# Performance work log

Hardware: AMD Instinct MI355X
Metric: run time of the kernel (lower is better)

Reference implementation:

```python
import jax, jax.numpy as jnp
import numpy as np

N_NODES = 50000
N_EDGES = 800000
IN_FEATS = 128
H_FEATS = 32
HEADS = 4
OUT_FEATS = 32
OUT_HEADS = 1
NEG_SLOPE = 0.2


def setup_inputs() -> dict:
    key = jax.random.key(0)
    ks = jax.random.split(key, 20)
    s = 0.05
    return {
        "features": jax.random.normal(ks[0], (N_NODES, IN_FEATS), jnp.float32),
        "src": jax.random.randint(ks[1], (N_EDGES,), 0, N_NODES, jnp.int32),
        "dst": jax.random.randint(ks[2], (N_EDGES,), 0, N_NODES, jnp.int32),
        "Ws0": jax.random.normal(ks[3], (IN_FEATS, HEADS * H_FEATS), jnp.float32) * s,
        "bs0": jnp.zeros((HEADS * H_FEATS,), jnp.float32),
        "Wd0": jax.random.normal(ks[4], (IN_FEATS, HEADS * H_FEATS), jnp.float32) * s,
        "bd0": jnp.zeros((HEADS * H_FEATS,), jnp.float32),
        "a0": jax.random.normal(ks[5], (HEADS, H_FEATS), jnp.float32) * s,
        "Ws1": jax.random.normal(ks[6], (HEADS * H_FEATS, HEADS * H_FEATS), jnp.float32) * s,
        "bs1": jnp.zeros((HEADS * H_FEATS,), jnp.float32),
        "Wd1": jax.random.normal(ks[7], (HEADS * H_FEATS, HEADS * H_FEATS), jnp.float32) * s,
        "bd1": jnp.zeros((HEADS * H_FEATS,), jnp.float32),
        "a1": jax.random.normal(ks[8], (HEADS, H_FEATS), jnp.float32) * s,
        "Ws2": jax.random.normal(ks[9], (HEADS * H_FEATS, OUT_HEADS * OUT_FEATS), jnp.float32) * s,
        "bs2": jnp.zeros((OUT_HEADS * OUT_FEATS,), jnp.float32),
        "Wd2": jax.random.normal(ks[10], (HEADS * H_FEATS, OUT_HEADS * OUT_FEATS), jnp.float32) * s,
        "bd2": jnp.zeros((OUT_HEADS * OUT_FEATS,), jnp.float32),
        "a2": jax.random.normal(ks[11], (OUT_HEADS, OUT_FEATS), jnp.float32) * s,
    }


def gatv2_conv(x, src, dst, Ws, bs, Wd, bd, attn, n_nodes):
    """DGL GATv2Conv (share_weights=False, residual=False, no dropout)."""
    heads, f = attn.shape
    feat_src = (x @ Ws + bs).reshape(-1, heads, f)  # [N, H, F]
    feat_dst = (x @ Wd + bd).reshape(-1, heads, f)  # [N, H, F]
    # per-edge GATv2 score: LeakyReLU(Wsrc h_u + Wdst h_v) . a
    e = jax.nn.leaky_relu(feat_src[src] + feat_dst[dst], NEG_SLOPE)  # [E, H, F]
    logits = jnp.einsum("ehf,hf->eh", e, attn)  # [E, H]
    # edge softmax over incoming edges of each dst node
    m = jax.ops.segment_max(logits, dst, num_segments=n_nodes)  # [N, H]
    ex = jnp.exp(logits - m[dst])
    denom = jax.ops.segment_sum(ex, dst, num_segments=n_nodes)  # [N, H]
    alpha = ex / denom[dst]  # [E, H]
    # scatter-aggregate messages
    msg = feat_src[src] * alpha[..., None]  # [E, H, F]
    return jax.ops.segment_sum(msg, dst, num_segments=n_nodes)  # [N, H, F]


def reference(features, src, dst,
              Ws0, bs0, Wd0, bd0, a0,
              Ws1, bs1, Wd1, bd1, a1,
              Ws2, bs2, Wd2, bd2, a2):
    n = features.shape[0]
    h = gatv2_conv(features, src, dst, Ws0, bs0, Wd0, bd0, a0, n)
    h = jax.nn.relu(h.reshape(n, -1))
    h = gatv2_conv(h, src, dst, Ws1, bs1, Wd1, bd1, a1, n)
    h = jax.nn.relu(h.reshape(n, -1))
    h = gatv2_conv(h, src, dst, Ws2, bs2, Wd2, bd2, a2, n)
    return h.mean(axis=1)  # [N, OUT_FEATS]
```

## Files before the change

### kernel.cpp

```cpp
#include <hip/hip_runtime.h>

typedef __attribute__((ext_vector_type(8))) short bf16x8;
typedef __attribute__((ext_vector_type(4))) float f32x4;

#define LOG2E 1.4426950408889634f

#define BINSH 8
#define NBIN 196
#define CHUNK 4096
#define K4CAP 6144

__device__ __forceinline__ unsigned bf_rn(float f) {
    unsigned u = __float_as_uint(f);
    u += 0x7fffu + ((u >> 16) & 1u);
    return u >> 16;
}
__device__ __forceinline__ float bf_lo(unsigned u) { return __uint_as_float(u << 16); }
__device__ __forceinline__ float bf_hi(unsigned u) { return __uint_as_float(u & 0xffff0000u); }

template <int CTRL>
__device__ __forceinline__ float dpp_radd(float x) {
    int t = __builtin_amdgcn_update_dpp(0, __float_as_int(x), CTRL, 0xF, 0xF, true);
    return x + __int_as_float(t);
}
__device__ __forceinline__ float sum8(float p) {
    p = dpp_radd<0x141>(p);
    p = dpp_radd<0x1B>(p);
    p = dpp_radd<0xB1>(p);
    return p;
}
__device__ __forceinline__ float sum4(float p) {
    p = dpp_radd<0xB1>(p);
    p = dpp_radd<0x4E>(p);
    return p;
}
__device__ __forceinline__ float dpp_swap1(float x) {
    return __int_as_float(__builtin_amdgcn_update_dpp(0, __float_as_int(x), 0xB1, 0xF, 0xF, true));
}

__device__ __forceinline__ float fast_exp2(float x) {
#if __has_builtin(__builtin_amdgcn_exp2f)
    return __builtin_amdgcn_exp2f(x);
#else
    return __expf(x * 0.6931471805599453f);
#endif
}


__global__ __launch_bounds__(256) void bin_count(const int* __restrict__ dst,
                                                 int* __restrict__ binCnt, int e) {
    __shared__ int hist[NBIN];
    for (int t = threadIdx.x; t < NBIN; t += 256) hist[t] = 0;
    __syncthreads();
    int base = blockIdx.x * CHUNK;
    int cnt = min(CHUNK, e - base);
    for (int j = threadIdx.x; j < cnt; j += 256)
        atomicAdd(&hist[dst[base + j] >> BINSH], 1);
    __syncthreads();
    for (int t = threadIdx.x; t < NBIN; t += 256)
        if (hist[t]) atomicAdd(&binCnt[t], hist[t]);
}

__global__ void bin_scan(const int* __restrict__ binCnt, int* __restrict__ binBase,
                         int* __restrict__ binCur, int* __restrict__ rowp, int n, int e) {
    int t = threadIdx.x;
    int v = (t < NBIN) ? binCnt[t] : 0;
    int lane = t & 63, w = t >> 6;
    int incl = v;
    for (int off = 1; off < 64; off <<= 1) {
        int tt = __shfl_up(incl, off);
        if (lane >= off) incl += tt;
    }
    __shared__ int wsum[4];
    if (lane == 63) wsum[w] = incl;
    __syncthreads();
    int wpre = 0;
    for (int i = 0; i < w; ++i) wpre += wsum[i];
    int excl = wpre + incl - v;
    if (t < NBIN) { binBase[t] = excl; binCur[t] = excl; }
    if (t == 0) { binBase[NBIN] = e; rowp[n] = e; }
}

__global__ __launch_bounds__(256) void bin_scatter(
    const int* __restrict__ src, const int* __restrict__ dst,
    int* __restrict__ binCur, unsigned* __restrict__ ebin, int e) {
    __shared__ int hist[256];
    __shared__ int seg[256];
    __shared__ int gbase[NBIN];
    __shared__ unsigned pack[CHUNK];
    for (int t = threadIdx.x; t < 256; t += 256) hist[t] = 0;
    __syncthreads();
    int base = blockIdx.x * CHUNK;
    int cnt = min(CHUNK, e - base);

    for (int j = threadIdx.x; j < cnt; j += 256)
        atomicAdd(&hist[dst[base + j] >> BINSH], 1);
    __syncthreads();
    if (threadIdx.x < 64) {
        int l = threadIdx.x;
        int s = 0, loc[4];
#pragma unroll
        for (int k = 0; k < 4; ++k) { loc[k] = s; s += hist[l * 4 + k]; }
        int incl = s;
        for (int off = 1; off < 64; off <<= 1) {
            int tt = __shfl_up(incl, off);
            if (l >= off) incl += tt;
        }
        int excl = incl - s;
#pragma unroll
        for (int k = 0; k < 4; ++k) seg[l * 4 + k] = excl + loc[k];
    }
    __syncthreads();
    if (threadIdx.x < NBIN && hist[threadIdx.x])
        gbase[threadIdx.x] = atomicAdd(&binCur[threadIdx.x], hist[threadIdx.x]);
    __syncthreads();
    for (int t = threadIdx.x; t < 256; t += 256) hist[t] = seg[t];
    __syncthreads();
    for (int j = threadIdx.x; j < cnt; j += 256) {
        int d = dst[base + j], s = src[base + j];
        int b = d >> BINSH, dl = d & ((1 << BINSH) - 1);
        int pos = atomicAdd(&hist[b], 1);
        pack[pos] = ((unsigned)b << 24) | ((unsigned)dl << 16) | (unsigned)s;
    }
    __syncthreads();
    for (int j = threadIdx.x; j < cnt; j += 256) {
        unsigned wv = pack[j];
        int b = wv >> 24;
        ebin[gbase[b] + (j - seg[b])] = wv;
    }
}

__global__ __launch_bounds__(256) void csr_build(
    const unsigned* __restrict__ ebin, const int* __restrict__ binBase,
    int* __restrict__ rowp, int* __restrict__ csrc, int n) {
    __shared__ int hist[256];
    __shared__ int seg[256];
    __shared__ unsigned stage[K4CAP];
    int b = blockIdx.x;
    int e0 = binBase[b], e1 = binBase[b + 1];
    int n0 = b << BINSH;
    int nn = min(256, n - n0);
    for (int t = threadIdx.x; t < 256; t += 256) hist[t] = 0;
    __syncthreads();
    for (int i = e0 + threadIdx.x; i < e1; i += 256) {
        unsigned wv = ebin[i];
        atomicAdd(&hist[(wv >> 16) & 255], 1);
        int off = i - e0;
        if (off < K4CAP) stage[off] = wv;
    }
    __syncthreads();
    if (threadIdx.x < 64) {
        int l = threadIdx.x;
        int s = 0, loc[4];
#pragma unroll
        for (int k = 0; k < 4; ++k) { loc[k] = s; s += hist[l * 4 + k]; }
        int incl = s;
        for (int off = 1; off < 64; off <<= 1) {
            int tt = __shfl_up(incl, off);
            if (l >= off) incl += tt;
        }
        int excl = incl - s;
#pragma unroll
        for (int k = 0; k < 4; ++k) seg[l * 4 + k] = excl + loc[k];
    }
    __syncthreads();
    for (int t = threadIdx.x; t < nn; t += 256) rowp[n0 + t] = e0 + seg[t];
    for (int t = threadIdx.x; t < 256; t += 256) hist[t] = seg[t];
    __syncthreads();
    for (int i = e0 + threadIdx.x; i < e1; i += 256) {
        int off = i - e0;
        unsigned wv = (off < K4CAP) ? stage[off] : ebin[i];
        int dl = (wv >> 16) & 255;
        int pos = e0 + atomicAdd(&hist[dl], 1);
        csrc[pos] = (int)(wv & 0xFFFFu);
    }
}


__global__ __launch_bounds__(256) void prep(
    const float* __restrict__ x, unsigned short* __restrict__ xb, int n4,
    const float* __restrict__ Ws0, const float* __restrict__ Wd0,
    const float* __restrict__ Ws1, const float* __restrict__ Wd1,
    const float* __restrict__ Ws2, const float* __restrict__ Wd2,
    unsigned short* __restrict__ wt0, unsigned short* __restrict__ wt1,
    unsigned short* __restrict__ wt2, int* __restrict__ binCnt) {
    int gid = blockIdx.x * blockDim.x + threadIdx.x;
    if (gid < NBIN) binCnt[gid] = 0;
    if (gid < n4) {
        float4 v = *(const float4*)(x + (size_t)gid * 4);
        ushort4 r;
        r.x = (unsigned short)bf_rn(v.x); r.y = (unsigned short)bf_rn(v.y);
        r.z = (unsigned short)bf_rn(v.z); r.w = (unsigned short)bf_rn(v.w);
        *(ushort4*)(xb + (size_t)gid * 4) = r;
    } else {
        int g = gid - n4;
        if (g < 65536) {
            int l = g >> 15, loc = g & 32767;
            int c = loc >> 7, k = loc & 127;
            const float* W = (c < 128) ? (l ? Ws1 : Ws0) : (l ? Wd1 : Wd0);
            int cc = c & 127;
            float v = W[(size_t)k * 128 + cc];
            (l ? wt1 : wt0)[loc] = (unsigned short)bf_rn(v);
        } else if (g < 65536 + 8192) {
            int loc = g - 65536;
            int c = loc >> 7, k = loc & 127;
            const float* W = (c < 32) ? Ws2 : Wd2;
            int cc = (c < 32) ? c : c - 32;
            float v = W[(size_t)k * 32 + cc];
            wt2[loc] = (unsigned short)bf_rn(v);
        }
    }
}


template <int COLS2>
__global__ __launch_bounds__(256) void gemm_dual2(
    const unsigned short* __restrict__ xb, const unsigned short* __restrict__ wt,
    const float* __restrict__ bs, const float* __restrict__ bd,
    unsigned short* __restrict__ fs, unsigned short* __restrict__ fd,
    int n, int nch) {
    constexpr int C  = COLS2 / 2;
    constexpr int NC = COLS2 / 64;

    const int lane = threadIdx.x & 63;
    const int m = lane & 15, quad = lane >> 4;
    const int gwid = blockIdx.x * 4 + (threadIdx.x >> 6);
    const int nwaves = gridDim.x * 4;
    const int cs = gwid % NC;
    const int cstride = nwaves / NC;

    float biasv[4];
#pragma unroll
    for (int ct = 0; ct < 4; ++ct) {
        int col = cs * 64 + ct * 16 + m;
        biasv[ct] = (col < C) ? bs[col] : bd[col - C];
    }

    for (int chunk = gwid / NC; chunk < nch; chunk += cstride) {
        const size_t r0 = (size_t)chunk * 64;

        f32x4 acc[4][4];
#pragma unroll
        for (int rt = 0; rt < 4; ++rt)
#pragma unroll
            for (int ct = 0; ct < 4; ++ct) acc[rt][ct] = (f32x4){0.f, 0.f, 0.f, 0.f};

#pragma unroll
        for (int ks = 0; ks < 4; ++ks) {
            const int ko = ks * 32 + quad * 8;
            bf16x8 a[4], b[4];
#pragma unroll
            for (int rt = 0; rt < 4; ++rt)
                a[rt] = *(const bf16x8*)(xb + (r0 + rt * 16 + m) * 128 + ko);
#pragma unroll
            for (int ct = 0; ct < 4; ++ct)
                b[ct] = *(const bf16x8*)(wt + (size_t)(cs * 64 + ct * 16 + m) * 128 + ko);
#pragma unroll
            for (int rt = 0; rt < 4; ++rt)
#pragma unroll
                for (int ct = 0; ct < 4; ++ct)
                    acc[rt][ct] = __builtin_amdgcn_mfma_f32_16x16x32_bf16(a[rt], b[ct], acc[rt][ct], 0, 0, 0);
        }

        const int odd = m & 1;
#pragma unroll
        for (int ct = 0; ct < 4; ++ct) {
            int colE = cs * 64 + ct * 16 + (m & ~1);
            unsigned short* ptr = (colE < C) ? fs : fd;
            int cc = (colE < C) ? colE : colE - C;
#pragma unroll
            for (int rt = 0; rt < 4; ++rt) {
                float v0 = acc[rt][ct][0] + biasv[ct];
                float v1 = acc[rt][ct][1] + biasv[ct];
                float v2 = acc[rt][ct][2] + biasv[ct];
                float v3 = acc[rt][ct][3] + biasv[ct];
                float s0 = dpp_swap1(v0), s1 = dpp_swap1(v1);
                float s2 = dpp_swap1(v2), s3 = dpp_swap1(v3);
                float aLo = odd ? s2 : v0, aHi = odd ? v2 : s0;
                float bLo = odd ? s3 : v1, bHi = odd ? v3 : s1;
                int rowA = (int)r0 + rt * 16 + quad * 4 + (odd ? 2 : 0);
                unsigned pa = (bf_rn(aHi) << 16) | bf_rn(aLo);
                unsigned pb = (bf_rn(bHi) << 16) | bf_rn(bLo);
                if (rowA < n)     *(unsigned*)(ptr + (size_t)rowA * C + cc)       = pa;
                if (rowA + 1 < n) *(unsigned*)(ptr + ((size_t)rowA + 1) * C + cc) = pb;
            }
        }
    }
}


#define EDGE_BODY(u, mval)                                          \
    do {                                                            \
        float x0 = bf_lo((u).x), x1 = bf_hi((u).x);                 \
        float x2 = bf_lo((u).y), x3 = bf_hi((u).y);                 \
        float t0 = x0 + fd0, t1 = x1 + fd1;                         \
        float t2 = x2 + fd2, t3 = x3 + fd3;                         \
        float p = a060 * t0;                                        \
        p = fmaf(a040, fabsf(t0), p);                               \
        p = fmaf(a061, t1, p); p = fmaf(a041, fabsf(t1), p);        \
        p = fmaf(a062, t2, p); p = fmaf(a042, fabsf(t2), p);        \
        p = fmaf(a063, t3, p); p = fmaf(a043, fabsf(t3), p);        \
        p = sum8(p);                                                \
        float ex = fast_exp2(p) * (mval);                           \
        denom += ex;                                                \
        acc0 = fmaf(ex, x0, acc0); acc1 = fmaf(ex, x1, acc1);       \
        acc2 = fmaf(ex, x2, acc2); acc3 = fmaf(ex, x3, acc3);       \
    } while (0)

#define EB8(u, mval)                                                \
    do {                                                            \
        float x0 = bf_lo((u).x), x1 = bf_hi((u).x);                 \
        float x2 = bf_lo((u).y), x3 = bf_hi((u).y);                 \
        float x4 = bf_lo((u).z), x5 = bf_hi((u).z);                 \
        float x6 = bf_lo((u).w), x7 = bf_hi((u).w);                 \
        float t0 = x0 + fd0, t1 = x1 + fd1;                         \
        float t2 = x2 + fd2, t3 = x3 + fd3;                         \
        float t4 = x4 + fd4, t5 = x5 + fd5;                         \
        float t6 = x6 + fd6, t7 = x7 + fd7;                         \
        float p = a60_0 * t0;                                       \
        p = fmaf(a40_0, fabsf(t0), p);                              \
        p = fmaf(a60_1, t1, p); p = fmaf(a40_1, fabsf(t1), p);      \
        p = fmaf(a60_2, t2, p); p = fmaf(a40_2, fabsf(t2), p);      \
        p = fmaf(a60_3, t3, p); p = fmaf(a40_3, fabsf(t3), p);      \
        p = fmaf(a60_4, t4, p); p = fmaf(a40_4, fabsf(t4), p);      \
        p = fmaf(a60_5, t5, p); p = fmaf(a40_5, fabsf(t5), p);      \
        p = fmaf(a60_6, t6, p); p = fmaf(a40_6, fabsf(t6), p);      \
        p = fmaf(a60_7, t7, p); p = fmaf(a40_7, fabsf(t7), p);      \
        p = sum4(p);                                                \
        float ex = fast_exp2(p) * (mval);                           \
        denom += ex;                                                \
        acc0 = fmaf(ex, x0, acc0); acc1 = fmaf(ex, x1, acc1);       \
        acc2 = fmaf(ex, x2, acc2); acc3 = fmaf(ex, x3, acc3);       \
        acc4 = fmaf(ex, x4, acc4); acc5 = fmaf(ex, x5, acc5);       \
        acc6 = fmaf(ex, x6, acc6); acc7 = fmaf(ex, x7, acc7);       \
    } while (0)

__global__ __launch_bounds__(256) void conv128(
    const unsigned short* __restrict__ fs, const unsigned short* __restrict__ fd,
    const float* __restrict__ attn, const int* __restrict__ rowp,
    const int* __restrict__ csrc, unsigned short* __restrict__ out, int n) {
    const int nwaves = gridDim.x * 4;
    const int wid0 = blockIdx.x * 4 + (threadIdx.x >> 6);
    const int lane = threadIdx.x & 63;
    const int slot = lane >> 4;
    const int c = lane & 15;

    float4 av0 = *(const float4*)(attn + c * 8);
    float4 av1 = *(const float4*)(attn + c * 8 + 4);
    const float a60_0 = av0.x * 0.6f * LOG2E, a40_0 = av0.x * 0.4f * LOG2E;
    const float a60_1 = av0.y * 0.6f * LOG2E, a40_1 = av0.y * 0.4f * LOG2E;
    const float a60_2 = av0.z * 0.6f * LOG2E, a40_2 = av0.z * 0.4f * LOG2E;
    const float a60_3 = av0.w * 0.6f * LOG2E, a40_3 = av0.w * 0.4f * LOG2E;
    const float a60_4 = av1.x * 0.6f * LOG2E, a40_4 = av1.x * 0.4f * LOG2E;
    const float a60_5 = av1.y * 0.6f * LOG2E, a40_5 = av1.y * 0.4f * LOG2E;
    const float a60_6 = av1.z * 0.6f * LOG2E, a40_6 = av1.z * 0.4f * LOG2E;
    const float a60_7 = av1.w * 0.6f * LOG2E, a40_7 = av1.w * 0.4f * LOG2E;

    for (int wid = wid0; wid < n; wid += nwaves) {
        uint4 ud = *(const uint4*)(fd + (size_t)wid * 128 + c * 8);
        float fd0 = bf_lo(ud.x), fd1 = bf_hi(ud.x);
        float fd2 = bf_lo(ud.y), fd3 = bf_hi(ud.y);
        float fd4 = bf_lo(ud.z), fd5 = bf_hi(ud.z);
        float fd6 = bf_lo(ud.w), fd7 = bf_hi(ud.w);
        int rs = rowp[wid], re = rowp[wid + 1];
        float acc0 = 0.f, acc1 = 0.f, acc2 = 0.f, acc3 = 0.f;
        float acc4 = 0.f, acc5 = 0.f, acc6 = 0.f, acc7 = 0.f, denom = 0.f;

        int i = rs;
        for (; i + 7 < re; i += 8) {
            int sA = csrc[i + slot];
            int sB = csrc[i + 4 + slot];
            uint4 uA = *(const uint4*)(fs + ((size_t)sA << 7) + c * 8);
            uint4 uB = *(const uint4*)(fs + ((size_t)sB << 7) + c * 8);
            EB8(uA, 1.0f);
            EB8(uB, 1.0f);
        }
        for (; i + 3 < re; i += 4) {
            int s = csrc[i + slot];
            uint4 u = *(const uint4*)(fs + ((size_t)s << 7) + c * 8);
            EB8(u, 1.0f);
        }
        if (i < re) {
            int idx = i + slot;
            int s = csrc[min(idx, re - 1)];
            uint4 u = *(const uint4*)(fs + ((size_t)s << 7) + c * 8);
            float mval = (idx < re) ? 1.f : 0.f;
            EB8(u, mval);
        }
        acc0 += __shfl_xor(acc0, 16); acc1 += __shfl_xor(acc1, 16);
        acc2 += __shfl_xor(acc2, 16); acc3 += __shfl_xor(acc3, 16);
        acc4 += __shfl_xor(acc4, 16); acc5 += __shfl_xor(acc5, 16);
        acc6 += __shfl_xor(acc6, 16); acc7 += __shfl_xor(acc7, 16);
        denom += __shfl_xor(denom, 16);
        acc0 += __shfl_xor(acc0, 32); acc1 += __shfl_xor(acc1, 32);
        acc2 += __shfl_xor(acc2, 32); acc3 += __shfl_xor(acc3, 32);
        acc4 += __shfl_xor(acc4, 32); acc5 += __shfl_xor(acc5, 32);
        acc6 += __shfl_xor(acc6, 32); acc7 += __shfl_xor(acc7, 32);
        denom += __shfl_xor(denom, 32);
        float inv = (re > rs) ? 1.f / denom : 0.f;
        float r0 = fmaxf(acc0 * inv, 0.f), r1 = fmaxf(acc1 * inv, 0.f);
        float r2 = fmaxf(acc2 * inv, 0.f), r3 = fmaxf(acc3 * inv, 0.f);
        float r4 = fmaxf(acc4 * inv, 0.f), r5 = fmaxf(acc5 * inv, 0.f);
        float r6 = fmaxf(acc6 * inv, 0.f), r7 = fmaxf(acc7 * inv, 0.f);
        if (slot == 0) {
            uint4 o;
            o.x = (bf_rn(r1) << 16) | bf_rn(r0);
            o.y = (bf_rn(r3) << 16) | bf_rn(r2);
            o.z = (bf_rn(r5) << 16) | bf_rn(r4);
            o.w = (bf_rn(r7) << 16) | bf_rn(r6);
            *(uint4*)(out + (size_t)wid * 128 + c * 8) = o;
        }
    }
}

__global__ __launch_bounds__(256) void conv32(
    const unsigned short* __restrict__ fs, const unsigned short* __restrict__ fd,
    const float* __restrict__ attn, const int* __restrict__ rowp,
    const int* __restrict__ csrc, float* __restrict__ out, int n) {
    const int nwaves = gridDim.x * 4;
    const int wid0 = blockIdx.x * 4 + (threadIdx.x >> 6);
    const int lane = threadIdx.x & 63;
    const int g = lane >> 3;
    const int c = lane & 7;

    float4 av = *(const float4*)(attn + c * 4);
    const float a060 = av.x * 0.6f * LOG2E, a040 = av.x * 0.4f * LOG2E;
    const float a061 = av.y * 0.6f * LOG2E, a041 = av.y * 0.4f * LOG2E;
    const float a062 = av.z * 0.6f * LOG2E, a042 = av.z * 0.4f * LOG2E;
    const float a063 = av.w * 0.6f * LOG2E, a043 = av.w * 0.4f * LOG2E;

    for (int wid = wid0; wid < n; wid += nwaves) {
        uint2 ud = *(const uint2*)(fd + (size_t)wid * 32 + c * 4);
        float fd0 = bf_lo(ud.x), fd1 = bf_hi(ud.x);
        float fd2 = bf_lo(ud.y), fd3 = bf_hi(ud.y);
        int rs = rowp[wid], re = rowp[wid + 1];
        float acc0 = 0.f, acc1 = 0.f, acc2 = 0.f, acc3 = 0.f, denom = 0.f;

        int i = rs;
        for (; i + 15 < re; i += 16) {
            int s0 = csrc[i + g];
            int s1 = csrc[i + 8 + g];
            uint2 u0 = *(const uint2*)(fs + ((size_t)s0 << 5) + c * 4);
            uint2 u1 = *(const uint2*)(fs + ((size_t)s1 << 5) + c * 4);
            EDGE_BODY(u0, 1.0f);
            EDGE_BODY(u1, 1.0f);
        }
        for (; i + 7 < re; i += 8) {
            int s = csrc[i + g];
            uint2 u = *(const uint2*)(fs + ((size_t)s << 5) + c * 4);
            EDGE_BODY(u, 1.0f);
        }
        if (i < re) {
            int idx = i + g;
            int s = csrc[min(idx, re - 1)];
            uint2 u = *(const uint2*)(fs + ((size_t)s << 5) + c * 4);
            float mval = (idx < re) ? 1.f : 0.f;
            EDGE_BODY(u, mval);
        }
        acc0 = dpp_radd<0x128>(acc0); acc1 = dpp_radd<0x128>(acc1);
        acc2 = dpp_radd<0x128>(acc2); acc3 = dpp_radd<0x128>(acc3);
        denom = dpp_radd<0x128>(denom);
        acc0 += __shfl_xor(acc0, 16); acc1 += __shfl_xor(acc1, 16);
        acc2 += __shfl_xor(acc2, 16); acc3 += __shfl_xor(acc3, 16);
        denom += __shfl_xor(denom, 16);
        acc0 += __shfl_xor(acc0, 32); acc1 += __shfl_xor(acc1, 32);
        acc2 += __shfl_xor(acc2, 32); acc3 += __shfl_xor(acc3, 32);
        denom += __shfl_xor(denom, 32);
        float inv = (re > rs) ? 1.f / denom : 0.f;
        if (lane < 8) {
            float4 o;
            o.x = acc0 * inv; o.y = acc1 * inv;
            o.z = acc2 * inv; o.w = acc3 * inv;
            *(float4*)(out + (size_t)wid * 32 + c * 4) = o;
        }
    }
}


extern "C" void kernel_launch(void* const* d_in, const int* in_sizes, int n_in,
                              void* d_out, int out_size, void* d_ws, size_t ws_size,
                              hipStream_t stream) {
    const float* feats = (const float*)d_in[0];
    const int*   src   = (const int*)d_in[1];
    const int*   dst   = (const int*)d_in[2];
    const float* Ws0 = (const float*)d_in[3],  *bs0 = (const float*)d_in[4];
    const float* Wd0 = (const float*)d_in[5],  *bd0 = (const float*)d_in[6];
    const float* a0  = (const float*)d_in[7];
    const float* Ws1 = (const float*)d_in[8],  *bs1 = (const float*)d_in[9];
    const float* Wd1 = (const float*)d_in[10], *bd1 = (const float*)d_in[11];
    const float* a1  = (const float*)d_in[12];
    const float* Ws2 = (const float*)d_in[13], *bs2 = (const float*)d_in[14];
    const float* Wd2 = (const float*)d_in[15], *bd2 = (const float*)d_in[16];
    const float* a2  = (const float*)d_in[17];

    const int N = in_sizes[0] / 128;
    const int E = in_sizes[1];
    const int nch = (N + 63) / 64;
    const int NPAD = nch * 64;

    char* ws = (char*)d_ws;
    const size_t featB = (size_t)NPAD * 128 * 2;
    unsigned short* xb  = (unsigned short*)(ws);
    unsigned short* hb  = (unsigned short*)(ws + featB);
    unsigned short* fsb = (unsigned short*)(ws + 2 * featB);
    unsigned short* fdb = (unsigned short*)(ws + 3 * featB);
    char* p = ws + 4 * featB;
    unsigned short* wt0 = (unsigned short*)p; p += 256 * 128 * 2;
    unsigned short* wt1 = (unsigned short*)p; p += 256 * 128 * 2;
    unsigned short* wt2 = (unsigned short*)p; p += 64 * 128 * 2;
    int* rowp    = (int*)p;      p += ((size_t)(N + 1) * 4 + 255) / 256 * 256;
    int* binCnt  = (int*)p;      p += (NBIN * 4 + 255) / 256 * 256;
    int* binBase = (int*)p;      p += ((NBIN + 1) * 4 + 255) / 256 * 256;
    int* binCur  = (int*)p;      p += (NBIN * 4 + 255) / 256 * 256;
    unsigned* ebin = (unsigned*)p; p += (size_t)E * 4;
    int* csrc    = (int*)p;

    const int nchunks = (E + CHUNK - 1) / CHUNK;
    const int n4 = N * 128 / 4;

    prep<<<(n4 + 73728 + 255) / 256, 256, 0, stream>>>(
        feats, xb, n4, Ws0, Wd0, Ws1, Wd1, Ws2, Wd2, wt0, wt1, wt2, binCnt);

    bin_count<<<nchunks, 256, 0, stream>>>(dst, binCnt, E);
    bin_scan<<<1, 256, 0, stream>>>(binCnt, binBase, binCur, rowp, N, E);
    bin_scatter<<<nchunks, 256, 0, stream>>>(src, dst, binCur, ebin, E);
    csr_build<<<NBIN, 256, 0, stream>>>(ebin, binBase, rowp, csrc, N);

    const int g256 = nch;
    const int g64  = (nch + 3) / 4;
    const int convGrid = 2048;

    gemm_dual2<256><<<g256, 256, 0, stream>>>(xb, wt0, bs0, bd0, fsb, fdb, N, nch);
    conv128<<<convGrid, 256, 0, stream>>>(fsb, fdb, a0, rowp, csrc, hb, N);
    gemm_dual2<256><<<g256, 256, 0, stream>>>(hb, wt1, bs1, bd1, fsb, fdb, N, nch);
    conv128<<<convGrid, 256, 0, stream>>>(fsb, fdb, a1, rowp, csrc, hb, N);
    gemm_dual2<64><<<g64, 256, 0, stream>>>(hb, wt2, bs2, bd2, fsb, fdb, N, nch);
    conv32<<<convGrid, 256, 0, stream>>>(fsb, fdb, a2, rowp, csrc, (float*)d_out, N);
}
```

Baseline: 302.4 us.

## Software-pipeline gathers, use contiguous row ranges per wave, split score reduction

The 128-wide conv kernel now prefetches the next group of source-feature gathers before running the edge math on the current group, so gather latency overlaps with compute. Both conv kernels switch from a grid-stride row loop to contiguous row ranges per wave, which may improve locality of rowp, csrc and output accesses. The score dot product is split into two independent FMA chains to shorten the dependency chain. The costs are higher register pressure from the prefetched uint4 values and possible load imbalance, since each wave's rows can have very different degrees.

Measured after the change: 303.2 us. No clear change (+0.3%).

```diff
diff --git a/kernel.cpp b/kernel.cpp
--- a/kernel.cpp
+++ b/kernel.cpp
@@ -317,16 +317,17 @@
         float t2 = x2 + fd2, t3 = x3 + fd3;                         \
         float t4 = x4 + fd4, t5 = x5 + fd5;                         \
         float t6 = x6 + fd6, t7 = x7 + fd7;                         \
-        float p = a60_0 * t0;                                       \
-        p = fmaf(a40_0, fabsf(t0), p);                              \
-        p = fmaf(a60_1, t1, p); p = fmaf(a40_1, fabsf(t1), p);      \
-        p = fmaf(a60_2, t2, p); p = fmaf(a40_2, fabsf(t2), p);      \
-        p = fmaf(a60_3, t3, p); p = fmaf(a40_3, fabsf(t3), p);      \
-        p = fmaf(a60_4, t4, p); p = fmaf(a40_4, fabsf(t4), p);      \
-        p = fmaf(a60_5, t5, p); p = fmaf(a40_5, fabsf(t5), p);      \
-        p = fmaf(a60_6, t6, p); p = fmaf(a40_6, fabsf(t6), p);      \
-        p = fmaf(a60_7, t7, p); p = fmaf(a40_7, fabsf(t7), p);      \
-        p = sum4(p);                                                \
+        float p0 = a60_0 * t0;                                      \
+        p0 = fmaf(a40_0, fabsf(t0), p0);                            \
+        p0 = fmaf(a60_1, t1, p0); p0 = fmaf(a40_1, fabsf(t1), p0);  \
+        p0 = fmaf(a60_2, t2, p0); p0 = fmaf(a40_2, fabsf(t2), p0);  \
+        p0 = fmaf(a60_3, t3, p0); p0 = fmaf(a40_3, fabsf(t3), p0);  \
+        float p1 = a60_4 * t4;                                      \
+        p1 = fmaf(a40_4, fabsf(t4), p1);                            \
+        p1 = fmaf(a60_5, t5, p1); p1 = fmaf(a40_5, fabsf(t5), p1);  \
+        p1 = fmaf(a60_6, t6, p1); p1 = fmaf(a40_6, fabsf(t6), p1);  \
+        p1 = fmaf(a60_7, t7, p1); p1 = fmaf(a40_7, fabsf(t7), p1);  \
+        float p = sum4(p0 + p1);                                    \
         float ex = fast_exp2(p) * (mval);                           \
         denom += ex;                                                \
         acc0 = fmaf(ex, x0, acc0); acc1 = fmaf(ex, x1, acc1);       \
@@ -340,7 +341,7 @@
     const float* __restrict__ attn, const int* __restrict__ rowp,
     const int* __restrict__ csrc, unsigned short* __restrict__ out, int n) {
     const int nwaves = gridDim.x * 4;
-    const int wid0 = blockIdx.x * 4 + (threadIdx.x >> 6);
+    const int wid = blockIdx.x * 4 + (threadIdx.x >> 6);
     const int lane = threadIdx.x & 63;
     const int slot = lane >> 4;
     const int c = lane & 15;
@@ -356,34 +357,51 @@
     const float a60_6 = av1.z * 0.6f * LOG2E, a40_6 = av1.z * 0.4f * LOG2E;
     const float a60_7 = av1.w * 0.6f * LOG2E, a40_7 = av1.w * 0.4f * LOG2E;
 
-    for (int wid = wid0; wid < n; wid += nwaves) {
-        uint4 ud = *(const uint4*)(fd + (size_t)wid * 128 + c * 8);
+    const int q = n / nwaves, r = n % nwaves;
+    const int row0 = wid * q + min(wid, r);
+    const int row1 = row0 + q + (wid < r ? 1 : 0);
+
+    const unsigned short* fsc = fs + c * 8;
+
+    for (int row = row0; row < row1; ++row) {
+        uint4 ud = *(const uint4*)(fd + (size_t)row * 128 + c * 8);
         float fd0 = bf_lo(ud.x), fd1 = bf_hi(ud.x);
         float fd2 = bf_lo(ud.y), fd3 = bf_hi(ud.y);
         float fd4 = bf_lo(ud.z), fd5 = bf_hi(ud.z);
         float fd6 = bf_lo(ud.w), fd7 = bf_hi(ud.w);
-        int rs = rowp[wid], re = rowp[wid + 1];
+        int rs = rowp[row], re = rowp[row + 1];
         float acc0 = 0.f, acc1 = 0.f, acc2 = 0.f, acc3 = 0.f;
         float acc4 = 0.f, acc5 = 0.f, acc6 = 0.f, acc7 = 0.f, denom = 0.f;
 
         int i = rs;
-        for (; i + 7 < re; i += 8) {
-            int sA = csrc[i + slot];
-            int sB = csrc[i + 4 + slot];
-            uint4 uA = *(const uint4*)(fs + ((size_t)sA << 7) + c * 8);
-            uint4 uB = *(const uint4*)(fs + ((size_t)sB << 7) + c * 8);
-            EB8(uA, 1.0f);
-            EB8(uB, 1.0f);
+        const int ng = (re - rs) >> 3;
+        if (ng > 0) {
+            int ib = rs + 2 * slot;
+            int sA0 = csrc[ib], sA1 = csrc[ib + 1];
+            uint4 uA0 = *(const uint4*)(fsc + ((size_t)sA0 << 7));
+            uint4 uA1 = *(const uint4*)(fsc + ((size_t)sA1 << 7));
+            for (int g2 = 1; g2 < ng; ++g2) {
+                ib += 8;
+                int sB0 = csrc[ib], sB1 = csrc[ib + 1];
+                uint4 uB0 = *(const uint4*)(fsc + ((size_t)sB0 << 7));
+                uint4 uB1 = *(const uint4*)(fsc + ((size_t)sB1 << 7));
+                EB8(uA0, 1.0f);
+                EB8(uA1, 1.0f);
+                uA0 = uB0; uA1 = uB1;
+            }
+            EB8(uA0, 1.0f);
+            EB8(uA1, 1.0f);
+            i = rs + ng * 8;
         }
         for (; i + 3 < re; i += 4) {
             int s = csrc[i + slot];
-            uint4 u = *(const uint4*)(fs + ((size_t)s << 7) + c * 8);
+            uint4 u = *(const uint4*)(fsc + ((size_t)s << 7));
             EB8(u, 1.0f);
         }
         if (i < re) {
             int idx = i + slot;
             int s = csrc[min(idx, re - 1)];
-            uint4 u = *(const uint4*)(fs + ((size_t)s << 7) + c * 8);
+            uint4 u = *(const uint4*)(fsc + ((size_t)s << 7));
             float mval = (idx < re) ? 1.f : 0.f;
             EB8(u, mval);
         }
@@ -408,7 +426,7 @@
             o.y = (bf_rn(r3) << 16) | bf_rn(r2);
             o.z = (bf_rn(r5) << 16) | bf_rn(r4);
             o.w = (bf_rn(r7) << 16) | bf_rn(r6);
-            *(uint4*)(out + (size_t)wid * 128 + c * 8) = o;
+            *(uint4*)(out + (size_t)row * 128 + c * 8) = o;
         }
     }
 }
@@ -418,7 +436,7 @@
     const float* __restrict__ attn, const int* __restrict__ rowp,
     const int* __restrict__ csrc, float* __restrict__ out, int n) {
     const int nwaves = gridDim.x * 4;
-    const int wid0 = blockIdx.x * 4 + (threadIdx.x >> 6);
+    const int wid = blockIdx.x * 4 + (threadIdx.x >> 6);
     const int lane = threadIdx.x & 63;
     const int g = lane >> 3;
     const int c = lane & 7;
@@ -429,31 +447,37 @@
     const float a062 = av.z * 0.6f * LOG2E, a042 = av.z * 0.4f * LOG2E;
     const float a063 = av.w * 0.6f * LOG2E, a043 = av.w * 0.4f * LOG2E;
 
-    for (int wid = wid0; wid < n; wid += nwaves) {
-        uint2 ud = *(const uint2*)(fd + (size_t)wid * 32 + c * 4);
+    const int q = n / nwaves, r = n % nwaves;
+    const int row0 = wid * q + min(wid, r);
+    const int row1 = row0 + q + (wid < r ? 1 : 0);
+
+    const unsigned short* fsc = fs + c * 4;
+
+    for (int row = row0; row < row1; ++row) {
+        uint2 ud = *(const uint2*)(fd + (size_t)row * 32 + c * 4);
         float fd0 = bf_lo(ud.x), fd1 = bf_hi(ud.x);
         float fd2 = bf_lo(ud.y), fd3 = bf_hi(ud.y);
-        int rs = rowp[wid], re = rowp[wid + 1];
+        int rs = rowp[row], re = rowp[row + 1];
         float acc0 = 0.f, acc1 = 0.f, acc2 = 0.f, acc3 = 0.f, denom = 0.f;
 
         int i = rs;
         for (; i + 15 < re; i += 16) {
             int s0 = csrc[i + g];
             int s1 = csrc[i + 8 + g];
-            uint2 u0 = *(const uint2*)(fs + ((size_t)s0 << 5) + c * 4);
-            uint2 u1 = *(const uint2*)(fs + ((size_t)s1 << 5) + c * 4);
+            uint2 u0 = *(const uint2*)(fsc + ((size_t)s0 << 5));
+            uint2 u1 = *(const uint2*)(fsc + ((size_t)s1 << 5));
             EDGE_BODY(u0, 1.0f);
             EDGE_BODY(u1, 1.0f);
         }
         for (; i + 7 < re; i += 8) {
             int s = csrc[i + g];
-            uint2 u = *(const uint2*)(fs + ((size_t)s << 5) + c * 4);
+            uint2 u = *(const uint2*)(fsc + ((size_t)s << 5));
             EDGE_BODY(u, 1.0f);
         }
         if (i < re) {
             int idx = i + g;
             int s = csrc[min(idx, re - 1)];
-            uint2 u = *(const uint2*)(fs + ((size_t)s << 5) + c * 4);
+            uint2 u = *(const uint2*)(fsc + ((size_t)s << 5));
             float mval = (idx < re) ? 1.f : 0.f;
             EDGE_BODY(u, mval);
         }
@@ -471,7 +495,7 @@
             float4 o;
             o.x = acc0 * inv; o.y = acc1 * inv;
             o.z = acc2 * inv; o.w = acc3 * inv;
-            *(float4*)(out + (size_t)wid * 32 + c * 4) = o;
+            *(float4*)(out + (size_t)row * 32 + c * 4) = o;
         }
     }
 }
```
